# Optimization experiments

Measured on AMD Instinct MI355X. Metric: run time of the kernel, lower is better.

The kernel has to match this reference:

```python
import math
import jax, jax.numpy as jnp
import numpy as np

N_HEADS = 16
NUM_BUCKETS = 32
MAX_DISTANCE = 128
ROTARY_BASE = 10000.0


def rotate_half(x):
    x1, x2 = jnp.split(x, 2, axis=-1)
    return jnp.concatenate((-x2, x1), axis=-1)


def rotary_freqs(T, dim):
    inv_freq = 1.0 / (ROTARY_BASE ** (jnp.arange(0, dim, 2, dtype=jnp.float32) / dim))
    t = jnp.arange(T, dtype=jnp.float32)
    freqs = jnp.einsum('i,j->ij', t, inv_freq)  # [T, dim/2]
    return jnp.concatenate((freqs, freqs), axis=-1)  # [T, dim]


def rel_pos_bucket_causal(rel_pos, num_buckets=NUM_BUCKETS, max_distance=MAX_DISTANCE):
    n = jnp.maximum(-rel_pos, 0)  # [T, T] int
    max_exact = num_buckets // 2
    is_small = n < max_exact
    n_safe = jnp.maximum(n, 1).astype(jnp.float32)
    val_if_large = max_exact + (
        jnp.log(n_safe / max_exact) / math.log(max_distance / max_exact) * (num_buckets - max_exact)
    ).astype(jnp.int32)
    val_if_large = jnp.minimum(val_if_large, num_buckets - 1)
    return jnp.where(is_small, n, val_if_large)


def setup_inputs() -> dict:
    key = jax.random.key(0)
    ks = jax.random.split(key, 10)
    B, T, C = 2, 2048, 1024
    s = 0.02
    return {
        'x':  jax.random.normal(ks[0], (B, T, C), dtype=jnp.float32),
        'Wq': jax.random.normal(ks[1], (C, C), dtype=jnp.float32) * s,
        'bq': jnp.zeros((C,), dtype=jnp.float32),
        'Wk': jax.random.normal(ks[2], (C, C), dtype=jnp.float32) * s,
        'bk': jnp.zeros((C,), dtype=jnp.float32),
        'Wv': jax.random.normal(ks[3], (C, C), dtype=jnp.float32) * s,
        'bv': jnp.zeros((C,), dtype=jnp.float32),
        'Wp': jax.random.normal(ks[4], (C, C), dtype=jnp.float32) * s,
        'bp': jnp.zeros((C,), dtype=jnp.float32),
        'rel_bias_table': jax.random.normal(ks[5], (NUM_BUCKETS, N_HEADS), dtype=jnp.float32) * s,
    }


def reference(x, Wq, bq, Wk, bk, Wv, bv, Wp, bp, rel_bias_table):
    B, T, C = x.shape
    H = N_HEADS
    D = C // H

    def heads(y):
        return y.reshape(B, T, H, D).transpose(0, 2, 1, 3)  # [B,H,T,D]

    q = heads(x @ Wq + bq)
    k = heads(x @ Wk + bk)
    v = heads(x @ Wv + bv)

    # rotary (use_xpos=False -> scale=1)
    freqs = rotary_freqs(T, D)  # [T, D]
    cos, sin = jnp.cos(freqs), jnp.sin(freqs)
    q = q * cos + rotate_half(q) * sin
    k = k * cos + rotate_half(k) * sin

    # relative position bias (causal, scale=1.0)
    pos = jnp.arange(T)
    rel_pos = pos[None, :] - pos[:, None]  # k_pos - q_pos
    bucket = rel_pos_bucket_causal(rel_pos)  # [T, T]
    bias = rel_bias_table[bucket]  # [T, T, H]
    bias = bias.transpose(2, 0, 1)  # [H, T, T]

    att = jnp.einsum('bhid,bhjd->bhij', q, k) + bias[None]
    att = att * (1.0 / math.sqrt(D))
    causal = pos[None, :] <= pos[:, None]  # tril mask [T, T]
    att = jnp.where(causal[None, None], att, -jnp.inf)
    att = jax.nn.softmax(att, axis=-1)

    y = jnp.einsum('bhij,bhjd->bhid', att, v)  # [B,H,T,D]
    y = y.transpose(0, 2, 1, 3).reshape(B, T, C)
    return y @ Wp + bp
```

## Files before the change

### kernel.cpp

```cpp
#include <hip/hip_runtime.h>
#include <hip/hip_bf16.h>
#include <math.h>

#define B_ 2
#define T_ 2048
#define C_ 1024
#define H_ 16
#define D_ 64
#define M_ (B_ * T_)
#define K_ 1024

#define SCALE2 0.18033688011112043f

typedef short bf16x8 __attribute__((ext_vector_type(8)));
typedef float f32x4  __attribute__((ext_vector_type(4)));
typedef unsigned int u32;

__device__ __forceinline__ float u2f(unsigned short u) {
    union { unsigned int i; float f; } v; v.i = ((unsigned int)u) << 16; return v.f;
}
__device__ __forceinline__ unsigned short f2b(float f) {
    __hip_bfloat16 h = __float2bfloat16(f);
    return *reinterpret_cast<unsigned short*>(&h);
}
__device__ __forceinline__ u32 pack_bf16_rnd(float a, float b) {
    const u32 au = __float_as_uint(a) + 0x8000u;
    const u32 bu = __float_as_uint(b) + 0x8000u;
    return __builtin_amdgcn_perm(bu, au, 0x07060302u);
}
__device__ __forceinline__ void load_lds16(const void* g, void* l) {
    __builtin_amdgcn_global_load_lds(
        (const __attribute__((address_space(1))) u32*)g,
        (__attribute__((address_space(3))) u32*)l, 16, 0, 0);
}

__global__ __launch_bounds__(256) void prep(
    const float* __restrict__ x,
    const float* __restrict__ W0, const float* __restrict__ W1,
    const float* __restrict__ W2, const float* __restrict__ W3,
    const float* __restrict__ tbl,
    unsigned short* __restrict__ xb,
    unsigned short* __restrict__ T0, unsigned short* __restrict__ T1,
    unsigned short* __restrict__ T2, unsigned short* __restrict__ T3,
    float* __restrict__ dtab, float2* __restrict__ trig)
{
    __shared__ __align__(16) unsigned short tile[64][72];
    const int bx = blockIdx.x;
    const int tid = threadIdx.x;

    if (bx < 2048) {
        const int idx = bx * 256 + tid;
        const float4 a = reinterpret_cast<const float4*>(x)[idx * 2];
        const float4 b = reinterpret_cast<const float4*>(x)[idx * 2 + 1];
        unsigned short t[8] = {f2b(a.x), f2b(a.y), f2b(a.z), f2b(a.w),
                               f2b(b.x), f2b(b.y), f2b(b.z), f2b(b.w)};
        reinterpret_cast<bf16x8*>(xb)[idx] = *reinterpret_cast<const bf16x8*>(t);
    } else if (bx < 3072) {
        const int w = bx - 2048;
        const int z = w >> 8;
        const int rem = w & 255;
        const int k0 = (rem & 15) * 64, n0 = (rem >> 4) * 64;
        const float* W = z == 0 ? W0 : z == 1 ? W1 : z == 2 ? W2 : W3;
        unsigned short* Wt = z == 0 ? T0 : z == 1 ? T1 : z == 2 ? T2 : T3;

        #pragma unroll
        for (int it = 0; it < 4; ++it) {
            const int idx = it * 256 + tid;
            const int r = idx >> 4, c = (idx & 15) * 4;
            const float4 w4 = *reinterpret_cast<const float4*>(W + (size_t)(k0 + r) * C_ + n0 + c);
            tile[r][c + 0] = f2b(w4.x); tile[r][c + 1] = f2b(w4.y);
            tile[r][c + 2] = f2b(w4.z); tile[r][c + 3] = f2b(w4.w);
        }
        __syncthreads();
        #pragma unroll
        for (int it = 0; it < 2; ++it) {
            const int idx = it * 256 + tid;
            const int nc = idx >> 3, kc = (idx & 7) * 8;
            unsigned short tmp[8];
            #pragma unroll
            for (int e = 0; e < 8; ++e) tmp[e] = tile[kc + e][nc];
            *reinterpret_cast<bf16x8*>(Wt + (size_t)(n0 + nc) * K_ + k0 + kc) =
                *reinterpret_cast<const bf16x8*>(tmp);
        }
    } else {
        const int idx = (bx - 3072) * 256 + tid;
        if (idx < H_ * T_) {
            const int h = idx >> 11, n = idx & (T_ - 1);
            int bucket;
            if (n < 16) bucket = n;
            else {
                int vb = 16 + (int)(log2f((float)n * 0.0625f) * (16.0f / 3.0f));
                bucket = vb < 31 ? vb : 31;
            }
            dtab[idx] = tbl[bucket * H_ + h] * SCALE2;
        }
        const int t = idx >> 5, j = idx & 31;
        const float inv = exp2f(-(float)j * (13.287712379549449f / 32.0f));
        const float ang = (float)t * inv;
        trig[idx] = make_float2(cosf(ang), sinf(ang));
    }
}

__device__ __forceinline__ void gemm_core(
    const unsigned short* __restrict__ A, const unsigned short* __restrict__ Bt,
    const float* __restrict__ bias, const float2* __restrict__ trig,
    float rot_scale, float* __restrict__ outf,
    unsigned short* __restrict__ outb, int mode)
{
    __shared__ __align__(16) unsigned short As[128 * 32];
    __shared__ __align__(16) unsigned short Bs[128 * 32];

    const int tid = threadIdx.x;
    const int wid = tid >> 6, lane = tid & 63;
    const int l16 = lane & 15, quad = lane >> 4;
    const int wm = wid >> 1, wn = wid & 1;
    const int m0 = blockIdx.y * 128, n0 = blockIdx.x * 128;

    f32x4 acc[4][4];
    #pragma unroll
    for (int i = 0; i < 4; ++i)
        #pragma unroll
        for (int j = 0; j < 4; ++j) acc[i][j] = (f32x4){0.f, 0.f, 0.f, 0.f};

    char* AsB = (char*)As;
    char* BsB = (char*)Bs;

    for (int k0 = 0; k0 < K_; k0 += 32) {
        __syncthreads();
        #pragma unroll
        for (int it = 0; it < 2; ++it) {
            const int idx = it * 256 + tid;
            const int row = idx >> 2, ch = (idx & 3) * 8;
            const int ldso = it * 4096 + wid * 1024;
            load_lds16(A + (size_t)(m0 + row) * K_ + k0 + ch, AsB + ldso);
            load_lds16(Bt + (size_t)(n0 + row) * K_ + k0 + ch, BsB + ldso);
        }
        __syncthreads();

        bf16x8 af[4], bf[4];
        #pragma unroll
        for (int i = 0; i < 4; ++i) {
            af[i] = *reinterpret_cast<const bf16x8*>(&As[(wm * 64 + i * 16 + l16) * 32 + quad * 8]);
            bf[i] = *reinterpret_cast<const bf16x8*>(&Bs[(wn * 64 + i * 16 + l16) * 32 + quad * 8]);
        }
        #pragma unroll
        for (int i = 0; i < 4; ++i)
            #pragma unroll
            for (int j = 0; j < 4; ++j)
                acc[i][j] = __builtin_amdgcn_mfma_f32_16x16x32_bf16(af[i], bf[j], acc[i][j], 0, 0, 0);
    }

    if (mode == 1) {
        #pragma unroll
        for (int i = 0; i < 4; ++i) {
            const int mb = m0 + wm * 64 + i * 16 + quad * 4;
            const int bb = mb >> 11, tb = mb & (T_ - 1);
            #pragma unroll
            for (int jc = 0; jc < 2; ++jc) {
                const int n_lo = n0 + wn * 64 + jc * 16 + l16;
                const int h = n_lo >> 6, d = n_lo & 63;
                const float bv_lo = bias[n_lo], bv_hi = bias[n_lo + 32];
                unsigned short* po = outb + (((size_t)bb * H_ + h) * T_ + tb) * D_ + d;
                #pragma unroll
                for (int r = 0; r < 4; ++r) {
                    const float2 cs = trig[(tb + r) * 32 + d];
                    const float a = acc[i][jc][r] + bv_lo;
                    const float b = acc[i][jc + 2][r] + bv_hi;
                    po[(size_t)r * D_]      = f2b((a * cs.x - b * cs.y) * rot_scale);
                    po[(size_t)r * D_ + 32] = f2b((b * cs.x + a * cs.y) * rot_scale);
                }
            }
        }
        return;
    }

    #pragma unroll
    for (int i = 0; i < 4; ++i) {
        const int mb = m0 + wm * 64 + i * 16 + quad * 4;
        #pragma unroll
        for (int j = 0; j < 4; ++j) {
            const int n = n0 + wn * 64 + j * 16 + l16;
            const float bv = bias[n];
            if (mode == 2) {
                const int bb = mb >> 11, t = mb & (T_ - 1);
                const int h = n >> 6, d = n & 63;
                uint2 w;
                w.x = pack_bf16_rnd(acc[i][j][0] + bv, acc[i][j][1] + bv);
                w.y = pack_bf16_rnd(acc[i][j][2] + bv, acc[i][j][3] + bv);
                *reinterpret_cast<uint2*>(
                    outb + (((size_t)bb * H_ + h) * D_ + d) * T_ + t) = w;
            } else {
                #pragma unroll
                for (int r = 0; r < 4; ++r)
                    outf[(size_t)(mb + r) * C_ + n] = acc[i][j][r] + bv;
            }
        }
    }
}

__global__ __launch_bounds__(256) void gemm_qkv(
    const unsigned short* __restrict__ A,
    const unsigned short* __restrict__ Wq, const unsigned short* __restrict__ Wk,
    const unsigned short* __restrict__ Wv,
    const float* __restrict__ bq, const float* __restrict__ bk,
    const float* __restrict__ bv, const float2* __restrict__ trig,
    unsigned short* __restrict__ Qo, unsigned short* __restrict__ Ko,
    unsigned short* __restrict__ Vto)
{
    const int z = blockIdx.z;
    const unsigned short* Bt = z == 0 ? Wq : z == 1 ? Wk : Wv;
    const float* bias = z == 0 ? bq : z == 1 ? bk : bv;
    unsigned short* outb = z == 0 ? Qo : z == 1 ? Ko : Vto;
    const float rs = z == 0 ? SCALE2 : 1.0f;
    gemm_core(A, Bt, bias, trig, rs, nullptr, outb, z == 2 ? 2 : 1);
}

__global__ __launch_bounds__(256) void gemm_proj(
    const unsigned short* __restrict__ A, const unsigned short* __restrict__ Bt,
    const float* __restrict__ bias, float* __restrict__ outf)
{
    gemm_core(A, Bt, bias, nullptr, 1.0f, outf, nullptr, 0);
}

__global__ __launch_bounds__(256) void flash_attn(
    const unsigned short* __restrict__ Q, const unsigned short* __restrict__ K,
    const unsigned short* __restrict__ Vt, const float* __restrict__ dtab,
    unsigned short* __restrict__ Y)
{
    __shared__ __align__(16) unsigned short Ks[64][72];
    __shared__ __align__(16) unsigned short Vs[64][72];
    __shared__ __align__(16) unsigned short Ps[4][16][72];
    __shared__ __align__(16) float bias_ls[64 + T_];

    const int bh = blockIdx.y;
    const int h = bh & (H_ - 1), b = bh >> 4;
    const int tid = threadIdx.x;
    const int wid = tid >> 6, lane = tid & 63;
    const int l16 = lane & 15, quad = lane >> 4;
    const size_t base = (size_t)bh * T_ * D_;
    const size_t vbase = (size_t)bh * D_ * T_;

    const int qta = (int)((blockIdx.x + blockIdx.y) & 15);
    const int qtb = 31 - qta;

    if (tid < 64) bias_ls[tid] = -INFINITY;
    for (int ii = tid; ii < qtb * 64 + 64; ii += 256) bias_ls[64 + ii] = dtab[h * T_ + ii];

    bf16x8 ones;
    #pragma unroll
    for (int e = 0; e < 8; ++e) ones[e] = (short)0x3F80;

    const int sr0 = tid >> 3,         sch0 = (tid & 7) * 8;
    const int sr1 = (tid + 256) >> 3, sch1 = ((tid + 256) & 7) * 8;

    bf16x8 kr[2], vr[2];
    kr[0] = *reinterpret_cast<const bf16x8*>(K + base + (size_t)sr0 * D_ + sch0);
    kr[1] = *reinterpret_cast<const bf16x8*>(K + base + (size_t)sr1 * D_ + sch1);
    vr[0] = *reinterpret_cast<const bf16x8*>(Vt + vbase + (size_t)sr0 * T_ + sch0);
    vr[1] = *reinterpret_cast<const bf16x8*>(Vt + vbase + (size_t)sr1 * T_ + sch1);

    for (int qi = 0; qi < 2; ++qi) {
        const int qt = qi ? qta : qtb;
        const int q0 = qt * 64;
        const int arow = q0 + wid * 16 + l16;
        const int crow = q0 + wid * 16 + quad * 4;
        const int nbase = crow - l16 * 4;

        bf16x8 qf[2];
        qf[0] = *reinterpret_cast<const bf16x8*>(Q + base + (size_t)arow * D_ + quad * 8);
        qf[1] = *reinterpret_cast<const bf16x8*>(Q + base + (size_t)arow * D_ + 32 + quad * 8);

        f32x4 o[4], ol;
        #pragma unroll
        for (int c = 0; c < 4; ++c) o[c] = (f32x4){0.f, 0.f, 0.f, 0.f};
        ol = (f32x4){0.f, 0.f, 0.f, 0.f};

        for (int kt = 0; kt <= qt; ++kt) {
            const int j0 = kt * 64;
            __syncthreads();

            *reinterpret_cast<bf16x8*>(&Ks[sr0][sch0]) = kr[0];
            *reinterpret_cast<bf16x8*>(&Ks[sr1][sch1]) = kr[1];
            *reinterpret_cast<bf16x8*>(&Vs[sr0][sch0]) = vr[0];
            *reinterpret_cast<bf16x8*>(&Vs[sr1][sch1]) = vr[1];
            __syncthreads();

            if (kt < qt) {
                const int j1 = j0 + 64;
                kr[0] = *reinterpret_cast<const bf16x8*>(K + base + (size_t)(j1 + sr0) * D_ + sch0);
                kr[1] = *reinterpret_cast<const bf16x8*>(K + base + (size_t)(j1 + sr1) * D_ + sch1);
                vr[0] = *reinterpret_cast<const bf16x8*>(Vt + vbase + (size_t)sr0 * T_ + j1 + sch0);
                vr[1] = *reinterpret_cast<const bf16x8*>(Vt + vbase + (size_t)sr1 * T_ + j1 + sch1);
            } else if (qi == 0) {
                kr[0] = *reinterpret_cast<const bf16x8*>(K + base + (size_t)sr0 * D_ + sch0);
                kr[1] = *reinterpret_cast<const bf16x8*>(K + base + (size_t)sr1 * D_ + sch1);
                vr[0] = *reinterpret_cast<const bf16x8*>(Vt + vbase + (size_t)sr0 * T_ + sch0);
                vr[1] = *reinterpret_cast<const bf16x8*>(Vt + vbase + (size_t)sr1 * T_ + sch1);
            }

            const int d0 = nbase - j0;
            const f32x4 blo = *reinterpret_cast<const f32x4*>(&bias_ls[60 + d0]);
            const f32x4 bhi = *reinterpret_cast<const f32x4*>(&bias_ls[64 + d0]);

            f32x4 sc[4];
            #pragma unroll
            for (int c = 0; c < 4; ++c) {
                #pragma unroll
                for (int r = 0; r < 4; ++r)
                    sc[c][r] = (r >= c) ? bhi[r - c] : blo[4 + r - c];
            }
            __builtin_amdgcn_s_setprio(1);
            #pragma unroll
            for (int c = 0; c < 4; ++c) {
                #pragma unroll
                for (int s = 0; s < 2; ++s) {
                    bf16x8 kf = *reinterpret_cast<const bf16x8*>(
                        &Ks[l16 * 4 + c][s * 32 + quad * 8]);
                    sc[c] = __builtin_amdgcn_mfma_f32_16x16x32_bf16(qf[s], kf, sc[c], 0, 0, 0);
                }
            }
            __builtin_amdgcn_s_setprio(0);

            #pragma unroll
            for (int r = 0; r < 4; ++r) {
                const float p0 = exp2f(sc[0][r]);
                const float p1 = exp2f(sc[1][r]);
                const float p2 = exp2f(sc[2][r]);
                const float p3 = exp2f(sc[3][r]);
                uint2 w;
                w.x = pack_bf16_rnd(p0, p1);
                w.y = pack_bf16_rnd(p2, p3);
                *reinterpret_cast<uint2*>(&Ps[wid][quad * 4 + r][l16 * 4]) = w;
            }

            __builtin_amdgcn_s_setprio(1);
            #pragma unroll
            for (int s = 0; s < 2; ++s) {
                bf16x8 pf = *reinterpret_cast<const bf16x8*>(&Ps[wid][l16][s * 32 + quad * 8]);
                #pragma unroll
                for (int c = 0; c < 4; ++c) {
                    bf16x8 vf = *reinterpret_cast<const bf16x8*>(&Vs[c * 16 + l16][s * 32 + quad * 8]);
                    o[c] = __builtin_amdgcn_mfma_f32_16x16x32_bf16(pf, vf, o[c], 0, 0, 0);
                }
                ol = __builtin_amdgcn_mfma_f32_16x16x32_bf16(pf, ones, ol, 0, 0, 0);
            }
            __builtin_amdgcn_s_setprio(0);
        }

        #pragma unroll
        for (int r = 0; r < 4; ++r) {
            const int i = crow + r;
            const float invl = 1.0f / ol[r];
            #pragma unroll
            for (int c = 0; c < 4; ++c)
                Y[((size_t)b * T_ + i) * C_ + h * D_ + c * 16 + l16] = f2b(o[c][r] * invl);
        }
    }
}

extern "C" void kernel_launch(void* const* d_in, const int* in_sizes, int n_in,
                              void* d_out, int out_size, void* d_ws, size_t ws_size,
                              hipStream_t stream)
{
    const float* x   = (const float*)d_in[0];
    const float* Wq  = (const float*)d_in[1];
    const float* bq  = (const float*)d_in[2];
    const float* Wk  = (const float*)d_in[3];
    const float* bk  = (const float*)d_in[4];
    const float* Wv  = (const float*)d_in[5];
    const float* bv  = (const float*)d_in[6];
    const float* Wp  = (const float*)d_in[7];
    const float* bp  = (const float*)d_in[8];
    const float* tbl = (const float*)d_in[9];
    float* out = (float*)d_out;

    const size_t n1 = (size_t)B_ * H_ * T_ * D_;
    const size_t nW = (size_t)C_ * C_;
    unsigned short* xb  = (unsigned short*)d_ws;
    unsigned short* Wqt = xb + (size_t)M_ * K_;
    unsigned short* Wkt = Wqt + nW;
    unsigned short* Wvt = Wkt + nW;
    unsigned short* Wpt = Wvt + nW;
    unsigned short* Qb  = Wpt + nW;
    unsigned short* Kb  = Qb + n1;
    unsigned short* Vtb = Kb + n1;
    unsigned short* Yb  = Vtb + n1;
    float* dtab = (float*)(Yb + n1);
    float2* trig = (float2*)(dtab + H_ * T_);

    const dim3 blk(256);

    prep<<<dim3(3328), blk, 0, stream>>>(x, Wq, Wk, Wv, Wp, tbl,
                                         xb, Wqt, Wkt, Wvt, Wpt, dtab, trig);

    gemm_qkv<<<dim3(C_ / 128, M_ / 128, 3), blk, 0, stream>>>(
        xb, Wqt, Wkt, Wvt, bq, bk, bv, trig, Qb, Kb, Vtb);

    flash_attn<<<dim3(16, B_ * H_), blk, 0, stream>>>(Qb, Kb, Vtb, dtab, Yb);

    gemm_proj<<<dim3(C_ / 128, M_ / 128), blk, 0, stream>>>(Yb, Wpt, bp, out);
}
```

Measured before the change: 213.6 us.

## Double-buffer K/V shared tiles with one barrier per step and remap block indices

K and V tiles now sit in double-buffered LDS. Each step writes the next tile into the alternate buffer while computing on the current one, and prefetches the tile after that into registers. This removes one of the two barriers per key tile, and a flat schedule index spans both query tiles of the pair. The block-to-head mapping is linearised so consecutive blocks cover different heads, and exp2f is replaced by the hardware exp2 intrinsic. The cost is doubled K/V LDS use, which may reduce occupancy.

```diff
diff --git a/kernel.cpp b/kernel.cpp
--- a/kernel.cpp
+++ b/kernel.cpp
@@ -227,12 +227,14 @@
     const unsigned short* __restrict__ Vt, const float* __restrict__ dtab,
     unsigned short* __restrict__ Y)
 {
-    __shared__ __align__(16) unsigned short Ks[64][72];
-    __shared__ __align__(16) unsigned short Vs[64][72];
+    __shared__ __align__(16) unsigned short Ks[2][64][72];
+    __shared__ __align__(16) unsigned short Vs[2][64][72];
     __shared__ __align__(16) unsigned short Ps[4][16][72];
     __shared__ __align__(16) float bias_ls[64 + T_];
 
-    const int bh = blockIdx.y;
+    const int lin = (int)(blockIdx.y * gridDim.x + blockIdx.x);
+    const int bh  = lin & 31;
+    const int rem = lin >> 5;
     const int h = bh & (H_ - 1), b = bh >> 4;
     const int tid = threadIdx.x;
     const int wid = tid >> 6, lane = tid & 63;
@@ -240,7 +242,7 @@
     const size_t base = (size_t)bh * T_ * D_;
     const size_t vbase = (size_t)bh * D_ * T_;
 
-    const int qta = (int)((blockIdx.x + blockIdx.y) & 15);
+    const int qta = (rem + bh) & 15;
     const int qtb = 31 - qta;
 
     if (tid < 64) bias_ls[tid] = -INFINITY;
@@ -258,7 +260,17 @@
     kr[1] = *reinterpret_cast<const bf16x8*>(K + base + (size_t)sr1 * D_ + sch1);
     vr[0] = *reinterpret_cast<const bf16x8*>(Vt + vbase + (size_t)sr0 * T_ + sch0);
     vr[1] = *reinterpret_cast<const bf16x8*>(Vt + vbase + (size_t)sr1 * T_ + sch1);
-
+    *reinterpret_cast<bf16x8*>(&Ks[0][sr0][sch0]) = kr[0];
+    *reinterpret_cast<bf16x8*>(&Ks[0][sr1][sch1]) = kr[1];
+    *reinterpret_cast<bf16x8*>(&Vs[0][sr0][sch0]) = vr[0];
+    *reinterpret_cast<bf16x8*>(&Vs[0][sr1][sch1]) = vr[1];
+    kr[0] = *reinterpret_cast<const bf16x8*>(K + base + (size_t)(64 + sr0) * D_ + sch0);
+    kr[1] = *reinterpret_cast<const bf16x8*>(K + base + (size_t)(64 + sr1) * D_ + sch1);
+    vr[0] = *reinterpret_cast<const bf16x8*>(Vt + vbase + (size_t)sr0 * T_ + 64 + sch0);
+    vr[1] = *reinterpret_cast<const bf16x8*>(Vt + vbase + (size_t)sr1 * T_ + 64 + sch1);
+    __syncthreads();
+
+    int t = 0;
     for (int qi = 0; qi < 2; ++qi) {
         const int qt = qi ? qta : qtb;
         const int q0 = qt * 64;
@@ -275,27 +287,23 @@
         for (int c = 0; c < 4; ++c) o[c] = (f32x4){0.f, 0.f, 0.f, 0.f};
         ol = (f32x4){0.f, 0.f, 0.f, 0.f};
 
-        for (int kt = 0; kt <= qt; ++kt) {
+        for (int kt = 0; kt <= qt; ++kt, ++t) {
             const int j0 = kt * 64;
-            __syncthreads();
-
-            *reinterpret_cast<bf16x8*>(&Ks[sr0][sch0]) = kr[0];
-            *reinterpret_cast<bf16x8*>(&Ks[sr1][sch1]) = kr[1];
-            *reinterpret_cast<bf16x8*>(&Vs[sr0][sch0]) = vr[0];
-            *reinterpret_cast<bf16x8*>(&Vs[sr1][sch1]) = vr[1];
-            __syncthreads();
-
-            if (kt < qt) {
-                const int j1 = j0 + 64;
-                kr[0] = *reinterpret_cast<const bf16x8*>(K + base + (size_t)(j1 + sr0) * D_ + sch0);
-                kr[1] = *reinterpret_cast<const bf16x8*>(K + base + (size_t)(j1 + sr1) * D_ + sch1);
-                vr[0] = *reinterpret_cast<const bf16x8*>(Vt + vbase + (size_t)sr0 * T_ + j1 + sch0);
-                vr[1] = *reinterpret_cast<const bf16x8*>(Vt + vbase + (size_t)sr1 * T_ + j1 + sch1);
-            } else if (qi == 0) {
-                kr[0] = *reinterpret_cast<const bf16x8*>(K + base + (size_t)sr0 * D_ + sch0);
-                kr[1] = *reinterpret_cast<const bf16x8*>(K + base + (size_t)sr1 * D_ + sch1);
-                vr[0] = *reinterpret_cast<const bf16x8*>(Vt + vbase + (size_t)sr0 * T_ + sch0);
-                vr[1] = *reinterpret_cast<const bf16x8*>(Vt + vbase + (size_t)sr1 * T_ + sch1);
+            const int cur = t & 1, nxt = cur ^ 1;
+
+            if (t < 32) {
+                *reinterpret_cast<bf16x8*>(&Ks[nxt][sr0][sch0]) = kr[0];
+                *reinterpret_cast<bf16x8*>(&Ks[nxt][sr1][sch1]) = kr[1];
+                *reinterpret_cast<bf16x8*>(&Vs[nxt][sr0][sch0]) = vr[0];
+                *reinterpret_cast<bf16x8*>(&Vs[nxt][sr1][sch1]) = vr[1];
+            }
+            if (t < 31) {
+                const int tn = t + 2;
+                const int jn = (tn <= qtb ? tn : tn - qtb - 1) * 64;
+                kr[0] = *reinterpret_cast<const bf16x8*>(K + base + (size_t)(jn + sr0) * D_ + sch0);
+                kr[1] = *reinterpret_cast<const bf16x8*>(K + base + (size_t)(jn + sr1) * D_ + sch1);
+                vr[0] = *reinterpret_cast<const bf16x8*>(Vt + vbase + (size_t)sr0 * T_ + jn + sch0);
+                vr[1] = *reinterpret_cast<const bf16x8*>(Vt + vbase + (size_t)sr1 * T_ + jn + sch1);
             }
 
             const int d0 = nbase - j0;
@@ -315,7 +323,7 @@
                 #pragma unroll
                 for (int s = 0; s < 2; ++s) {
                     bf16x8 kf = *reinterpret_cast<const bf16x8*>(
-                        &Ks[l16 * 4 + c][s * 32 + quad * 8]);
+                        &Ks[cur][l16 * 4 + c][s * 32 + quad * 8]);
                     sc[c] = __builtin_amdgcn_mfma_f32_16x16x32_bf16(qf[s], kf, sc[c], 0, 0, 0);
                 }
             }
@@ -323,10 +331,10 @@
 
             #pragma unroll
             for (int r = 0; r < 4; ++r) {
-                const float p0 = exp2f(sc[0][r]);
-                const float p1 = exp2f(sc[1][r]);
-                const float p2 = exp2f(sc[2][r]);
-                const float p3 = exp2f(sc[3][r]);
+                const float p0 = __builtin_amdgcn_exp2f(sc[0][r]);
+                const float p1 = __builtin_amdgcn_exp2f(sc[1][r]);
+                const float p2 = __builtin_amdgcn_exp2f(sc[2][r]);
+                const float p3 = __builtin_amdgcn_exp2f(sc[3][r]);
                 uint2 w;
                 w.x = pack_bf16_rnd(p0, p1);
                 w.y = pack_bf16_rnd(p2, p3);
@@ -339,12 +347,14 @@
                 bf16x8 pf = *reinterpret_cast<const bf16x8*>(&Ps[wid][l16][s * 32 + quad * 8]);
                 #pragma unroll
                 for (int c = 0; c < 4; ++c) {
-                    bf16x8 vf = *reinterpret_cast<const bf16x8*>(&Vs[c * 16 + l16][s * 32 + quad * 8]);
+                    bf16x8 vf = *reinterpret_cast<const bf16x8*>(&Vs[cur][c * 16 + l16][s * 32 + quad * 8]);
                     o[c] = __builtin_amdgcn_mfma_f32_16x16x32_bf16(pf, vf, o[c], 0, 0, 0);
                 }
                 ol = __builtin_amdgcn_mfma_f32_16x16x32_bf16(pf, ones, ol, 0, 0, 0);
             }
             __builtin_amdgcn_s_setprio(0);
+
+            __syncthreads();
         }
 
         #pragma unroll
```

Result: faster. 207.4 us (-2.9%).
